# Performance work log

Hardware: AMD Instinct MI355X
Metric: run time of the kernel (lower is better)

## Reference

```python
import jax, jax.numpy as jnp
import numpy as np

IN_F = 4096
OUT_F = 4096
B, S = 4, 2048
BITS = 4
N_LEVELS = 1 << BITS  # 16


def setup_inputs() -> dict:
    key = jax.random.key(0)
    kx, kr, ks, kb = jax.random.split(key, 4)
    x = jax.random.normal(kx, (B, S, IN_F), dtype=jnp.float32)
    # random orthogonal rotation (TurboQuantMSE rotation matrix, seeded)
    g = jax.random.normal(kr, (IN_F, IN_F), dtype=jnp.float32)
    rotation, _ = jnp.linalg.qr(g)
    # 4-bit scalar codebook: Lloyd-Max-style Gaussian levels, scaled for
    # unit-norm rows whose rotated entries ~ N(0, 1/in_features)
    p = (jnp.arange(N_LEVELS, dtype=jnp.float32) + 0.5) / N_LEVELS
    levels = jnp.sqrt(2.0) * jax.scipy.special.erfinv(2.0 * p - 1.0)
    codebook = (levels / jnp.sqrt(jnp.float32(IN_F))).astype(jnp.float32)
    weight_indices = jax.random.randint(jax.random.fold_in(key, 1), (OUT_F, IN_F), 0, N_LEVELS, dtype=jnp.int32)
    weight_scale = jax.random.uniform(ks, (OUT_F,), dtype=jnp.float32, minval=0.5, maxval=2.0)
    bias = jax.random.normal(kb, (OUT_F,), dtype=jnp.float32)
    return {"x": x, "weight_indices": weight_indices, "weight_scale": weight_scale,
            "bias": bias, "rotation": rotation, "codebook": codebook}


def reference(x, weight_indices, weight_scale, bias, rotation, codebook):
    # dequantize: codebook lookup -> inverse rotation -> per-row rescale
    w_rot = codebook[weight_indices]                      # (out, in)
    w_hat = jnp.einsum('oi,ji->oj', w_rot, rotation)      # apply R^T: (out, in)
    w = w_hat * weight_scale[:, None]                     # (out, in)
    # F.linear: x @ W^T + b
    return jnp.einsum('bsi,oi->bso', x, w) + bias
```

## Files before the change

### kernel.cpp

```cpp
#include <hip/hip_runtime.h>

typedef short short8 __attribute__((ext_vector_type(8)));
typedef float f32x4 __attribute__((ext_vector_type(4)));

#define GLOBAL_AS __attribute__((address_space(1)))
#define LDS_AS    __attribute__((address_space(3)))

__device__ __forceinline__ unsigned short f2bf(float f) {
    unsigned u = __builtin_bit_cast(unsigned, f);
    u += 0x7fffu + ((u >> 16) & 1u);
    return (unsigned short)(u >> 16);
}

__global__ __launch_bounds__(256) void k_convert_all(
        const int* __restrict__ widx, const float* __restrict__ cb,
        ushort* __restrict__ wq,
        const float* __restrict__ rot, ushort* __restrict__ rbuf,
        const float* __restrict__ x, ushort* __restrict__ xb) {
    const int N0 = 4194304, N1 = 4194304, N2 = 8388608;
    const int total = N0 + N1 + N2;
    const int stride = gridDim.x * 256;
    for (int i = blockIdx.x * 256 + threadIdx.x; i < total; i += stride) {
        if (i < N0) {
            int4 v = reinterpret_cast<const int4*>(widx)[i];
            ushort4 o;
            o.x = f2bf(cb[v.x]); o.y = f2bf(cb[v.y]);
            o.z = f2bf(cb[v.z]); o.w = f2bf(cb[v.w]);
            reinterpret_cast<ushort4*>(wq)[i] = o;
        } else if (i < N0 + N1) {
            int j = i - N0;
            float4 v = reinterpret_cast<const float4*>(rot)[j];
            ushort4 o;
            o.x = f2bf(v.x); o.y = f2bf(v.y); o.z = f2bf(v.z); o.w = f2bf(v.w);
            reinterpret_cast<ushort4*>(rbuf)[j] = o;
        } else {
            int j = i - N0 - N1;
            float4 v = reinterpret_cast<const float4*>(x)[j];
            ushort4 o;
            o.x = f2bf(v.x); o.y = f2bf(v.y); o.z = f2bf(v.z); o.w = f2bf(v.w);
            reinterpret_cast<ushort4*>(xb)[j] = o;
        }
    }
}


#define CH_AE(j) ((((j) & 8) << 1) | ((j) & 7))
#define CH_AL(j) (CH_AE(j) + 8)
#define CH_BE(j) ((((j) & 12) << 1) | ((j) & 3))
#define CH_BL(j) (CH_BE(j) + 4)

#define STAGE2(GB, LW, KB, CF) do {                                             \
    const int c0_ = CF(2 * w);                                                  \
    const int c1_ = CF(2 * w + 1);                                              \
    __builtin_amdgcn_global_load_lds(                                           \
        (const GLOBAL_AS void*)((GB) + (size_t)c0_ * 32768 + (KB)),             \
        (LDS_AS void*)((LW) + c0_ * 512), 16, 0, 0);                            \
    __builtin_amdgcn_global_load_lds(                                           \
        (const GLOBAL_AS void*)((GB) + (size_t)c1_ * 32768 + (KB)),             \
        (LDS_AS void*)((LW) + c1_ * 512), 16, 0, 0);                            \
} while (0)

#define READ_A(DST, BUF, MH) do {                                               \
    _Pragma("unroll")                                                           \
    for (int mi = 0; mi < 4; ++mi)                                              \
        DST[0][mi] = *reinterpret_cast<const short8*>(                          \
            sAc + ak0 + ((BUF) * 32768 + (MH) * 8192 + mi * 2048));             \
    _Pragma("unroll")                                                           \
    for (int mi = 0; mi < 4; ++mi)                                              \
        DST[1][mi] = *reinterpret_cast<const short8*>(                          \
            sAc + ak1 + ((BUF) * 32768 + (MH) * 8192 + mi * 2048));             \
} while (0)

#define READ_B(DST, BUF, NH) do {                                               \
    _Pragma("unroll")                                                           \
    for (int ni = 0; ni < 2; ++ni)                                              \
        DST[0][ni] = *reinterpret_cast<const short8*>(                          \
            sBc + bk0 + ((BUF) * 32768 + (NH) * 4096 + ni * 2048));             \
    _Pragma("unroll")                                                           \
    for (int ni = 0; ni < 2; ++ni)                                              \
        DST[1][ni] = *reinterpret_cast<const short8*>(                          \
            sBc + bk1 + ((BUF) * 32768 + (NH) * 4096 + ni * 2048));             \
} while (0)

#define MFMA_Q(MH, NH, K2, MI_B, MI_E, BF)                                      \
    _Pragma("unroll")                                                           \
    for (int mi = (MI_B); mi < (MI_E); ++mi)                                    \
        _Pragma("unroll")                                                       \
        for (int ni = 0; ni < 2; ++ni)                                          \
            acc[(MH) * 4 + mi][(NH) * 2 + ni] =                                 \
                __builtin_amdgcn_mfma_f32_16x16x32_bf16(                        \
                    aF[K2][mi], BF[K2][ni], acc[(MH) * 4 + mi][(NH) * 2 + ni], 0, 0, 0)

#define LG(N) do {                                                              \
    asm volatile("s_waitcnt lgkmcnt(" #N ")" ::: "memory");                     \
    __builtin_amdgcn_sched_barrier(0);                                          \
} while (0)

#define PHTOP do {                                                              \
    asm volatile("" ::: "memory");                                              \
    __builtin_amdgcn_s_barrier();                                               \
} while (0)

#define PH_END do {                                                             \
    __builtin_amdgcn_s_setprio(0);                                              \
    asm volatile("" ::: "memory");                                              \
    __builtin_amdgcn_s_barrier();                                               \
    asm volatile("" ::: "memory");                                              \
} while (0)

#define PH1S(BUF, ...) do {                                                     \
    READ_B(b0f, BUF, 0); READ_A(aF, BUF, 0);                                    \
    __VA_ARGS__;                                                                \
    asm volatile("s_waitcnt lgkmcnt(8)" ::: "memory");                          \
    PHTOP;                                                                      \
    LG(6); __builtin_amdgcn_s_setprio(1);                                       \
    MFMA_Q(0, 0, 0, 0, 2, b0f);                                                 \
    LG(4);                                                                      \
    MFMA_Q(0, 0, 0, 2, 4, b0f);                                                 \
    LG(0);                                                                      \
    MFMA_Q(0, 0, 1, 0, 4, b0f);                                                 \
    PH_END;                                                                     \
} while (0)

#define PH2S(BUF, ...) do {                                                     \
    READ_B(b1f, BUF, 1);                                                        \
    __VA_ARGS__;                                                                \
    PHTOP;                                                                      \
    LG(2); __builtin_amdgcn_s_setprio(1);                                       \
    MFMA_Q(0, 1, 0, 0, 4, b1f);                                                 \
    LG(0);                                                                      \
    MFMA_Q(0, 1, 1, 0, 4, b1f);                                                 \
    PH_END;                                                                     \
} while (0)

#define PH3S(BUF, ...) do {                                                     \
    READ_A(aF, BUF, 1);                                                         \
    __VA_ARGS__;                                                                \
    PHTOP;                                                                      \
    LG(4); __builtin_amdgcn_s_setprio(1);                                       \
    MFMA_Q(1, 0, 0, 0, 4, b0f);                                                 \
    LG(0);                                                                      \
    MFMA_Q(1, 0, 1, 0, 4, b0f);                                                 \
    PH_END;                                                                     \
} while (0)

#define PH4S(FN, ...) do {                                                      \
    __VA_ARGS__;                                                                \
    PHTOP;                                                                      \
    __builtin_amdgcn_s_setprio(1);                                              \
    MFMA_Q(1, 1, 0, 0, 4, b1f);                                                 \
    MFMA_Q(1, 1, 1, 0, 4, b1f);                                                 \
    __builtin_amdgcn_s_setprio(0);                                              \
    asm volatile("s_waitcnt vmcnt(" #FN ")" ::: "memory");                      \
    __builtin_amdgcn_s_barrier();                                               \
    asm volatile("" ::: "memory");                                              \
} while (0)

#define PH4SNF(...) do {                                                        \
    __VA_ARGS__;                                                                \
    PHTOP;                                                                      \
    __builtin_amdgcn_s_setprio(1);                                              \
    MFMA_Q(1, 1, 0, 0, 4, b1f);                                                 \
    MFMA_Q(1, 1, 1, 0, 4, b1f);                                                 \
    PH_END;                                                                     \
} while (0)

template <int EPI>
__global__ __launch_bounds__(512, 2) void gemm256(const ushort* __restrict__ A,
                                                  const ushort* __restrict__ B,
                                                  void* __restrict__ C,
                                                  const float* __restrict__ extra) {
    constexpr int K = 4096, N = 4096;
    __shared__ ushort sA[2][256 * 64];
    __shared__ ushort sB[2][256 * 64];

    const int tid  = threadIdx.x;
    const int w    = tid >> 6;
    const int lane = tid & 63;
    const int wm = w >> 2, wn = w & 3;

    const int nwg = gridDim.x;
    const int sw  = ((int)blockIdx.x & 7) * (nwg >> 3) + ((int)blockIdx.x >> 3);
    const int m0 = (sw >> 4) * 256;
    const int n0 = (sw & 15) * 256;

    const int srow8 = lane >> 3;
    const int scol  = (((lane & 7) ^ (lane >> 3)) * 8);
    const ushort* gAl = A + (size_t)m0 * K + srow8 * 4096 + scol;
    const ushort* gBl = B + (size_t)n0 * K + srow8 * 4096 + scol;

    const int fr   = lane & 15;
    const int fkb  = ((lane >> 4) & 3) * 16;
    const int swb  = (fr & 7) << 4;
    const int arow = wm * 128 + fr;
    const int brow = wn * 64 + fr;
    const char* sAc = (const char*)&sA[0][0];
    const char* sBc = (const char*)&sB[0][0];
    const int ak0 = (arow * 128 + 0  + fkb) ^ swb;
    const int ak1 = (arow * 128 + 64 + fkb) ^ swb;
    const int bk0 = (brow * 128 + 0  + fkb) ^ swb;
    const int bk1 = (brow * 128 + 64 + fkb) ^ swb;

    f32x4 acc[8][4];
#pragma unroll
    for (int i = 0; i < 8; ++i)
#pragma unroll
        for (int j = 0; j < 4; ++j) acc[i][j] = (f32x4){0.f, 0.f, 0.f, 0.f};

    short8 aF[2][4], b0f[2][2], b1f[2][2];

    STAGE2(gAl, sA[0], 0, CH_AE); STAGE2(gBl, sB[0], 0, CH_BE);
    STAGE2(gBl, sB[0], 0, CH_BL); STAGE2(gAl, sA[0], 0, CH_AL);
    STAGE2(gAl, sA[1], 64, CH_AE); STAGE2(gBl, sB[1], 64, CH_BE);
    STAGE2(gBl, sB[1], 64, CH_BL);
    asm volatile("s_waitcnt vmcnt(6)" ::: "memory");
    __builtin_amdgcn_s_barrier();
    asm volatile("" ::: "memory");

    for (int pr = 0; pr < 31; ++pr) {
        const int t = 2 * pr;
        const int kb1 = (t + 1) * 64, kb2 = (t + 2) * 64, kb3 = (t + 3) * 64;
        PH1S(0, STAGE2(gAl, sA[1], kb1, CH_AL));
        PH2S(0, STAGE2(gAl, sA[0], kb2, CH_AE));
        PH3S(0, STAGE2(gBl, sB[0], kb2, CH_BE));
        PH4S(6, STAGE2(gBl, sB[0], kb2, CH_BL));
        PH1S(1, STAGE2(gAl, sA[0], kb2, CH_AL));
        PH2S(1, STAGE2(gAl, sA[1], kb3, CH_AE));
        PH3S(1, STAGE2(gBl, sB[1], kb3, CH_BE));
        PH4S(6, STAGE2(gBl, sB[1], kb3, CH_BL));
    }
    {
        PH1S(0, STAGE2(gAl, sA[1], 63 * 64, CH_AL));
        PH2S(0, ((void)0));
        PH3S(0, ((void)0));
        PH4S(0, ((void)0));
        PH1S(1, ((void)0));
        PH2S(1, ((void)0));
        PH3S(1, ((void)0));
        PH4SNF(((void)0));
    }

    const int rb = m0 + wm * 128 + ((lane >> 4) * 4);
    const int cb = n0 + wn * 64 + (lane & 15);
    if (EPI == 0) {
        ushort* Cw = (ushort*)C;
#pragma unroll
        for (int mi = 0; mi < 8; ++mi) {
#pragma unroll
            for (int r = 0; r < 4; ++r) {
                const int row = rb + mi * 16 + r;
                const float s = extra[row];
#pragma unroll
                for (int ni = 0; ni < 4; ++ni)
                    Cw[(size_t)row * N + cb + ni * 16] = f2bf(acc[mi][ni][r] * s);
            }
        }
    } else {
        float* Cf = (float*)C;
#pragma unroll
        for (int ni = 0; ni < 4; ++ni) {
            const float b = extra[cb + ni * 16];
#pragma unroll
            for (int mi = 0; mi < 8; ++mi) {
#pragma unroll
                for (int r = 0; r < 4; ++r) {
                    const int row = rb + mi * 16 + r;
                    Cf[(size_t)row * N + cb + ni * 16] = acc[mi][ni][r] + b;
                }
            }
        }
    }
}

extern "C" void kernel_launch(void* const* d_in, const int* in_sizes, int n_in,
                              void* d_out, int out_size, void* d_ws, size_t ws_size,
                              hipStream_t stream) {
    const float* x     = (const float*)d_in[0];
    const int*   widx  = (const int*)  d_in[1];
    const float* wscal = (const float*)d_in[2];
    const float* bias  = (const float*)d_in[3];
    const float* rot   = (const float*)d_in[4];
    const float* cb    = (const float*)d_in[5];
    float* out = (float*)d_out;

    char* ws = (char*)d_ws;
    ushort* wq   = (ushort*)(ws);
    ushort* rbuf = (ushort*)(ws + 33554432);
    ushort* xb   = (ushort*)(ws + 67108864);
    ushort* wb   = (ushort*)(ws + 134217728);
    (void)ws_size; (void)in_sizes; (void)n_in; (void)out_size;

    k_convert_all<<<2048, 256, 0, stream>>>(widx, cb, wq, rot, rbuf, x, xb);

    gemm256<0><<<dim3(256), 512, 0, stream>>>(wq, rbuf, (void*)wb, wscal);

    gemm256<1><<<dim3(512), 512, 0, stream>>>(xb, wb, (void*)out, bias);
}
```

Baseline: 458.5 us.

## Prefetch next tile's B fragment in phase 4 and reorder stage loads

Restructures the 4-phase GEMM software pipeline so the B fragment for the next buffer is read from LDS during phase 4 of the previous tile instead of at the start of phase 1. Phase 1 then only loads A and waits on fewer LDS reads before its MFMAs. The global-to-LDS staging order is reshuffled so the buffer being overwritten matches the new read schedule, and the prologue now stages all four chunks with a full vmcnt(0) wait. Phase 4 gains an lgkmcnt(0) wait before the barrier, which may add stall, and the reordered staging changes how far global loads run ahead of use.

```diff
diff --git a/kernel.cpp b/kernel.cpp
--- a/kernel.cpp
+++ b/kernel.cpp
@@ -108,21 +108,18 @@
     asm volatile("" ::: "memory");                                              \
 } while (0)
 
-#define PH1S(BUF, ...) do {                                                     \
-    READ_B(b0f, BUF, 0); READ_A(aF, BUF, 0);                                    \
-    __VA_ARGS__;                                                                \
-    asm volatile("s_waitcnt lgkmcnt(8)" ::: "memory");                          \
-    PHTOP;                                                                      \
-    LG(6); __builtin_amdgcn_s_setprio(1);                                       \
-    MFMA_Q(0, 0, 0, 0, 2, b0f);                                                 \
-    LG(4);                                                                      \
-    MFMA_Q(0, 0, 0, 2, 4, b0f);                                                 \
+#define PH1N(BUF, ...) do {                                                     \
+    READ_A(aF, BUF, 0);                                                         \
+    __VA_ARGS__;                                                                \
+    PHTOP;                                                                      \
+    LG(4); __builtin_amdgcn_s_setprio(1);                                       \
+    MFMA_Q(0, 0, 0, 0, 4, b0f);                                                 \
     LG(0);                                                                      \
     MFMA_Q(0, 0, 1, 0, 4, b0f);                                                 \
     PH_END;                                                                     \
 } while (0)
 
-#define PH2S(BUF, ...) do {                                                     \
+#define PH2N(BUF, ...) do {                                                     \
     READ_B(b1f, BUF, 1);                                                        \
     __VA_ARGS__;                                                                \
     PHTOP;                                                                      \
@@ -133,7 +130,7 @@
     PH_END;                                                                     \
 } while (0)
 
-#define PH3S(BUF, ...) do {                                                     \
+#define PH3N(BUF, ...) do {                                                     \
     READ_A(aF, BUF, 1);                                                         \
     __VA_ARGS__;                                                                \
     PHTOP;                                                                      \
@@ -144,19 +141,21 @@
     PH_END;                                                                     \
 } while (0)
 
-#define PH4S(FN, ...) do {                                                      \
+#define PH4N(NBUF, FN, ...) do {                                                \
+    READ_B(b0f, NBUF, 0);                                                       \
     __VA_ARGS__;                                                                \
     PHTOP;                                                                      \
     __builtin_amdgcn_s_setprio(1);                                              \
     MFMA_Q(1, 1, 0, 0, 4, b1f);                                                 \
     MFMA_Q(1, 1, 1, 0, 4, b1f);                                                 \
     __builtin_amdgcn_s_setprio(0);                                              \
+    asm volatile("s_waitcnt lgkmcnt(0)" ::: "memory");                          \
     asm volatile("s_waitcnt vmcnt(" #FN ")" ::: "memory");                      \
     __builtin_amdgcn_s_barrier();                                               \
     asm volatile("" ::: "memory");                                              \
 } while (0)
 
-#define PH4SNF(...) do {                                                        \
+#define PH4E(...) do {                                                          \
     __VA_ARGS__;                                                                \
     PHTOP;                                                                      \
     __builtin_amdgcn_s_setprio(1);                                              \
@@ -212,32 +211,33 @@
     STAGE2(gAl, sA[0], 0, CH_AE); STAGE2(gBl, sB[0], 0, CH_BE);
     STAGE2(gBl, sB[0], 0, CH_BL); STAGE2(gAl, sA[0], 0, CH_AL);
     STAGE2(gAl, sA[1], 64, CH_AE); STAGE2(gBl, sB[1], 64, CH_BE);
-    STAGE2(gBl, sB[1], 64, CH_BL);
-    asm volatile("s_waitcnt vmcnt(6)" ::: "memory");
+    STAGE2(gBl, sB[1], 64, CH_BL); STAGE2(gAl, sA[1], 64, CH_AL);
+    asm volatile("s_waitcnt vmcnt(0)" ::: "memory");
     __builtin_amdgcn_s_barrier();
     asm volatile("" ::: "memory");
+    READ_B(b0f, 0, 0);
 
     for (int pr = 0; pr < 31; ++pr) {
         const int t = 2 * pr;
-        const int kb1 = (t + 1) * 64, kb2 = (t + 2) * 64, kb3 = (t + 3) * 64;
-        PH1S(0, STAGE2(gAl, sA[1], kb1, CH_AL));
-        PH2S(0, STAGE2(gAl, sA[0], kb2, CH_AE));
-        PH3S(0, STAGE2(gBl, sB[0], kb2, CH_BE));
-        PH4S(6, STAGE2(gBl, sB[0], kb2, CH_BL));
-        PH1S(1, STAGE2(gAl, sA[0], kb2, CH_AL));
-        PH2S(1, STAGE2(gAl, sA[1], kb3, CH_AE));
-        PH3S(1, STAGE2(gBl, sB[1], kb3, CH_BE));
-        PH4S(6, STAGE2(gBl, sB[1], kb3, CH_BL));
+        const int kb2 = (t + 2) * 64, kb3 = (t + 3) * 64;
+        PH1N(0,    STAGE2(gBl, sB[0], kb2, CH_BE));
+        PH2N(0,    STAGE2(gAl, sA[0], kb2, CH_AE));
+        PH3N(0,    STAGE2(gBl, sB[0], kb2, CH_BL));
+        PH4N(1, 6, STAGE2(gAl, sA[0], kb2, CH_AL));
+        PH1N(1,    STAGE2(gBl, sB[1], kb3, CH_BE));
+        PH2N(1,    STAGE2(gAl, sA[1], kb3, CH_AE));
+        PH3N(1,    STAGE2(gBl, sB[1], kb3, CH_BL));
+        PH4N(0, 6, STAGE2(gAl, sA[1], kb3, CH_AL));
     }
     {
-        PH1S(0, STAGE2(gAl, sA[1], 63 * 64, CH_AL));
-        PH2S(0, ((void)0));
-        PH3S(0, ((void)0));
-        PH4S(0, ((void)0));
-        PH1S(1, ((void)0));
-        PH2S(1, ((void)0));
-        PH3S(1, ((void)0));
-        PH4SNF(((void)0));
+        PH1N(0,    ((void)0));
+        PH2N(0,    ((void)0));
+        PH3N(0,    ((void)0));
+        PH4N(1, 0, ((void)0));
+        PH1N(1,    ((void)0));
+        PH2N(1,    ((void)0));
+        PH3N(1,    ((void)0));
+        PH4E(((void)0));
     }
 
     const int rb = m0 + wm * 128 + ((lane >> 4) * 4);
```

Result: slower. 531.1 us (+15.8%).
